# Optimization experiments

Hardware: AMD Instinct MI355X
Metric: run time of the kernel (lower is better)

## Reference

```python
import jax, jax.numpy as jnp
import numpy as np

N_NODES = 50000
N_EDGES = 800000
HEADS = 5
NFEAT = 5
C1 = 32  # hidden_layers


def setup_inputs() -> dict:
    key = jax.random.key(0)
    ks = jax.random.split(key, 20)
    s = 0.3  # glorot-ish scale
    d = {
        "x": jax.random.normal(ks[0], (N_NODES, NFEAT), jnp.float32),
        "edge_attr": jax.random.uniform(ks[1], (N_EDGES, 1), jnp.float32),
        "src": jax.random.randint(ks[2], (N_EDGES,), 0, N_NODES, jnp.int32),
        "dst": jax.random.randint(ks[3], (N_EDGES,), 0, N_NODES, jnp.int32),
        # conv1: in=5 -> heads=5, out=32, concat
        "W1": jax.random.normal(ks[4], (NFEAT, HEADS * C1), jnp.float32) * s,
        "a_src1": jax.random.normal(ks[5], (HEADS, C1), jnp.float32) * s,
        "a_dst1": jax.random.normal(ks[6], (HEADS, C1), jnp.float32) * s,
        "We1": jax.random.normal(ks[7], (1, HEADS * C1), jnp.float32) * s,
        "ae1": jax.random.normal(ks[8], (HEADS, C1), jnp.float32) * s,
        "b1": jnp.zeros((HEADS * C1,), jnp.float32),
        # conv2: in=160 -> heads=5, out=1, mean over heads
        "W2": jax.random.normal(ks[9], (HEADS * C1, HEADS * 1), jnp.float32) * 0.08,
        "a_src2": jax.random.normal(ks[10], (HEADS, 1), jnp.float32) * s,
        "a_dst2": jax.random.normal(ks[11], (HEADS, 1), jnp.float32) * s,
        "We2": jax.random.normal(ks[12], (1, HEADS * 1), jnp.float32) * s,
        "ae2": jax.random.normal(ks[13], (HEADS, 1), jnp.float32) * s,
        "b2": jnp.zeros((1,), jnp.float32),
        "Wlin": jax.random.normal(ks[14], (1, 1), jnp.float32),
    }
    return d


def gat_layer(x, src, dst, eattr, W, a_src, a_dst, We, a_e, bias, concat, n_nodes):
    """PyG GATConv with edge_dim, self-loops already added by caller."""
    H, C = a_src.shape
    h = (x @ W).reshape(-1, H, C)                      # [N,H,C]
    alpha_s = (h * a_src[None]).sum(-1)                # [N,H]
    alpha_d = (h * a_dst[None]).sum(-1)                # [N,H]
    ee = (eattr @ We).reshape(-1, H, C)                # [E,H,C]
    alpha_e = (ee * a_e[None]).sum(-1)                 # [E,H]
    logits = jax.nn.leaky_relu(alpha_s[src] + alpha_d[dst] + alpha_e, 0.2)
    # segment softmax over destination nodes
    m = jax.ops.segment_max(logits, dst, num_segments=n_nodes)
    m = jnp.where(jnp.isfinite(m), m, 0.0)
    ex = jnp.exp(logits - m[dst])
    denom = jax.ops.segment_sum(ex, dst, num_segments=n_nodes)
    alpha = ex / (denom[dst] + 1e-16)                  # [E,H]
    msg = (alpha[:, :, None] * h[src]).reshape(-1, H * C)
    agg = jax.ops.segment_sum(msg, dst, num_segments=n_nodes).reshape(n_nodes, H, C)
    if concat:
        return agg.reshape(n_nodes, H * C) + bias
    return agg.mean(axis=1) + bias


def reference(x, edge_attr, src, dst, W1, a_src1, a_dst1, We1, ae1, b1,
              W2, a_src2, a_dst2, We2, ae2, b2, Wlin):
    n = x.shape[0]
    loop = jnp.arange(n, dtype=src.dtype)
    s = jnp.concatenate([src, loop])
    t = jnp.concatenate([dst, loop])
    # self-loop edge_attr = mean of edge_attr (PyG fill_value='mean')
    ea_loop = jnp.broadcast_to(edge_attr.mean(axis=0, keepdims=True), (n, edge_attr.shape[1]))
    ea = jnp.concatenate([edge_attr, ea_loop], axis=0)

    x1 = gat_layer(x, s, t, ea, W1, a_src1, a_dst1, We1, ae1, b1, True, n)
    x2 = jax.nn.relu(x1)
    # dropout p=0.2 is identity in eval mode
    x4 = gat_layer(x2, s, t, ea, W2, a_src2, a_dst2, We2, ae2, b2, False, n)
    x5 = x4 @ Wlin                                     # Linear(1,1,bias=False)
    return jax.nn.sigmoid(x5)                          # [N,1]
```

## Files before the change

kernel.cpp:

```cpp
#include <hip/hip_runtime.h>
#include <hip/hip_fp16.h>
#include <math.h>

#define N_NODES 50000
#define N_EDGES 800000
#define E2 (N_EDGES + N_NODES)
#define HEADS 5
#define C1 32
#define F1 160

#define BSZ 64
#define NBK 782
#define NBL 128
#define CH  6641
#define MTOT (NBK*NBL)
#define MC  391
#define GRID_H1 (N_NODES/4)
#define CAP 1408

static constexpr size_t alignup(size_t x){ return (x + 255) & ~size_t(255); }
static constexpr size_t OFF_SCAL  = 0;
static constexpr size_t OFF_H     = alignup(OFF_SCAL + 64*4);
static constexpr size_t OFF_EAS   = alignup(OFF_H    + (size_t)MTOT*4);
static constexpr size_t OFF_PART  = alignup(OFF_EAS  + (size_t)NBL*4);
static constexpr size_t OFF_PPREF = alignup(OFF_PART + (size_t)MC*4);
static constexpr size_t OFF_BST   = alignup(OFF_PPREF+ (size_t)MC*4);
static constexpr size_t OFF_OFFS  = alignup(OFF_BST  + (size_t)(NBK+1)*4);
static constexpr size_t OFF_BPACK = alignup(OFF_OFFS + (size_t)(N_NODES+1)*4);
static constexpr size_t OFF_EDG   = alignup(OFF_BPACK+ (size_t)E2*8);
static constexpr size_t OFF_AS1P  = alignup(OFF_EDG  + (size_t)E2*4);
static constexpr size_t OFF_AD1P  = alignup(OFF_AS1P + (size_t)N_NODES*8*4);
static constexpr size_t OFF_G16   = alignup(OFF_AD1P + (size_t)N_NODES*8*4);
static constexpr size_t OFF_AD2P  = alignup(OFF_G16  + (size_t)N_NODES*16*2);
static constexpr size_t OFF_H1Q   = alignup(OFF_AD2P + (size_t)N_NODES*8*4);
static constexpr size_t OFF_X2H   = alignup(OFF_H1Q  + (size_t)N_NODES*F1);

typedef float vf2 __attribute__((ext_vector_type(2)));
__device__ __forceinline__ float4 fp8x4_to_f32(unsigned int r){
  vf2 lo = __builtin_amdgcn_cvt_pk_f32_fp8((int)r, false);
  vf2 hi = __builtin_amdgcn_cvt_pk_f32_fp8((int)r, true);
  return make_float4(lo.x, lo.y, hi.x, hi.y);
}

__global__ __launch_bounds__(320) void k_init(const float* __restrict__ x, const float* __restrict__ W1,
                       const float* __restrict__ as1w, const float* __restrict__ ad1w,
                       unsigned short* __restrict__ h1q, float* __restrict__ as1p, float* __restrict__ ad1p,
                       const int* __restrict__ dst, const float* __restrict__ ea,
                       int* __restrict__ H, float* __restrict__ easum){
  __shared__ float sW[5*F1];
  int t = threadIdx.x;
  if (blockIdx.x < GRID_H1){
    for (int k = t; k < 5*F1; k += 320) sW[k] = W1[k];
    __syncthreads();
    int nl = t / 80;
    int c  = t - nl*80;
    int n  = blockIdx.x*4 + nl;
    int c0 = 2*c;
    float hv0 = 0.f, hv1 = 0.f;
    #pragma unroll
    for (int f = 0; f < 5; f++){
      float xv = x[n*5 + f];
      hv0 += xv * sW[f*F1 + c0];
      hv1 += xv * sW[f*F1 + c0 + 1];
    }
    int pk = __builtin_amdgcn_cvt_pk_fp8_f32(hv0, hv1, 0, false);
    h1q[n*80 + c] = (unsigned short)(pk & 0xFFFF);
    float vs = hv0*as1w[c0] + hv1*as1w[c0+1];
    float vd = hv0*ad1w[c0] + hv1*ad1w[c0+1];
    #pragma unroll
    for (int m = 8; m >= 1; m >>= 1){
      vs += __shfl_xor(vs, m, 64);
      vd += __shfl_xor(vd, m, 64);
    }
    if ((c & 15) == 0){
      int h = c >> 4;
      as1p[n*8 + h] = vs;
      ad1p[n*8 + h] = vd;
    }
  } else {
    int* hist = (int*)sW;
    float* wsum = (float*)&hist[NBK + 1];
    for (int k = t; k < NBK; k += 320) hist[k] = 0;
    __syncthreads();
    int b = blockIdx.x - GRID_H1;
    int e0 = b*CH, e1 = min(e0 + CH, E2);
    float s = 0.f;
    for (int e = e0 + t; e < e1; e += 320){
      int d;
      if (e < N_EDGES){ d = dst[e]; s += ea[e]; }
      else d = e - N_EDGES;
      atomicAdd(&hist[d >> 6], 1);
    }
    #pragma unroll
    for (int m = 1; m < 64; m <<= 1) s += __shfl_xor(s, m, 64);
    if ((t & 63) == 0) wsum[t >> 6] = s;
    __syncthreads();
    for (int k = t; k < NBK; k += 320) H[(size_t)k*NBL + b] = hist[k];
    if (t == 0) easum[b] = wsum[0] + wsum[1] + wsum[2] + wsum[3] + wsum[4];
  }
}

__global__ void k_s1(const int* __restrict__ H, int* __restrict__ partial){
  int i = blockIdx.x*256 + threadIdx.x;
  int v = (i < MTOT) ? H[i] : 0;
  #pragma unroll
  for (int m = 1; m < 64; m <<= 1) v += __shfl_xor(v, m, 64);
  __shared__ int sh[4];
  if ((threadIdx.x & 63) == 0) sh[threadIdx.x >> 6] = v;
  __syncthreads();
  if (threadIdx.x == 0) partial[blockIdx.x] = sh[0] + sh[1] + sh[2] + sh[3];
}

__global__ __launch_bounds__(512) void k_s2p(const int* __restrict__ partial, int* __restrict__ ppref,
                      int* __restrict__ offs, int* __restrict__ bstart,
                      const float* __restrict__ easum,
                      const float* __restrict__ We1, const float* __restrict__ ae1,
                      const float* __restrict__ We2, const float* __restrict__ ae2,
                      float* __restrict__ scal){
  __shared__ int sp[512];
  __shared__ float sh_ea[NBL];
  int t = threadIdx.x;
  if (t < NBL) sh_ea[t] = easum[t];
  if (t >= 448 && t < 448 + HEADS){
    int h = t - 448;
    float s = 0.f;
    for (int c = 0; c < C1; c++) s += We1[h*C1 + c] * ae1[h*C1 + c];
    scal[2 + h] = s;
    scal[7 + h] = We2[h] * ae2[h];
  }
  int v = (t < MC) ? partial[t] : 0;
  sp[t] = v;
  __syncthreads();
  if (t == 511){
    float es = 0.f;
    for (int i = 0; i < NBL; i++) es += sh_ea[i];
    scal[1] = es / (float)N_EDGES;
  }
  for (int off = 1; off < 512; off <<= 1){
    int u = (t >= off) ? sp[t - off] : 0;
    __syncthreads();
    sp[t] += u;
    __syncthreads();
  }
  if (t < MC) ppref[t] = sp[t] - v;
  if (t == 0){ offs[N_NODES] = E2; bstart[NBK] = E2; }
}

__global__ void k_s3(int* __restrict__ H, const int* __restrict__ ppref, int* __restrict__ bstart){
  __shared__ int sp[256];
  int b = blockIdx.x, t = threadIdx.x;
  int i = b*256 + t;
  int v = (i < MTOT) ? H[i] : 0;
  sp[t] = v;
  __syncthreads();
  for (int off = 1; off < 256; off <<= 1){
    int u = (t >= off) ? sp[t - off] : 0;
    __syncthreads();
    sp[t] += u;
    __syncthreads();
  }
  int P = ppref[b] + sp[t] - v;
  if (i < MTOT){
    H[i] = P;
    if (i % NBL == 0) bstart[i / NBL] = P;
  }
}

__global__ __launch_bounds__(256) void k_scat(const int* __restrict__ src, const int* __restrict__ dst,
                       const float* __restrict__ ea, const float* __restrict__ scal,
                       const int* __restrict__ H, int2* __restrict__ bpack){
  __shared__ int lofs[NBK];
  int b = blockIdx.x;
  for (int k = threadIdx.x; k < NBK; k += 256) lofs[k] = H[(size_t)k*NBL + b];
  __syncthreads();
  float mean = scal[1];
  int e0 = b*CH, e1 = min(e0 + CH, E2);
  for (int e = e0 + threadIdx.x; e < e1; e += 256){
    int d, s; float a;
    if (e < N_EDGES){ d = dst[e]; s = src[e]; a = ea[e]; }
    else { d = s = e - N_EDGES; a = mean; }
    int pos = atomicAdd(&lofs[d >> 6], 1);
    bpack[pos] = make_int2(s | ((d & 63) << 16), __float_as_int(a));
  }
}

__global__ __launch_bounds__(256) void k_final2(const int* __restrict__ bstart,
                        const int2* __restrict__ bpack,
                        int* __restrict__ offs, unsigned int* __restrict__ edge2){
  __shared__ int cnt[BSZ], cur[BSZ];
  __shared__ unsigned int s_edge[CAP];
  int k = blockIdx.x, t = threadIdx.x;
  int base = k*BSZ;
  if (t < BSZ) cnt[t] = 0;
  __syncthreads();
  int r0 = bstart[k], r1 = bstart[k + 1];
  int sz = r1 - r0;
  for (int j = r0 + t; j < r1; j += 256) atomicAdd(&cnt[(bpack[j].x >> 16) & 63], 1);
  __syncthreads();
  if (t == 0){
    int run = 0;
    for (int i = 0; i < BSZ; i++){ int c = cnt[i]; cnt[i] = run; cur[i] = run; run += c; }
  }
  __syncthreads();
  if (t < BSZ){
    int n = base + t;
    if (n < N_NODES) offs[n] = r0 + cnt[t];
  }
  if (sz <= CAP){
    for (int j = r0 + t; j < r1; j += 256){
      int2 v = bpack[j];
      int lp = atomicAdd(&cur[(v.x >> 16) & 63], 1);
      s_edge[lp] = (unsigned int)(v.x & 0xFFFF) |
                   ((unsigned int)__half_as_ushort(__float2half(__int_as_float(v.y))) << 16);
    }
    __syncthreads();
    for (int i = t; i < sz; i += 256) edge2[r0 + i] = s_edge[i];
  } else {
    for (int j = r0 + t; j < r1; j += 256){
      int2 v = bpack[j];
      int pos = r0 + atomicAdd(&cur[(v.x >> 16) & 63], 1);
      edge2[pos] = (unsigned int)(v.x & 0xFFFF) |
                   ((unsigned int)__half_as_ushort(__float2half(__int_as_float(v.y))) << 16);
    }
  }
}

__global__ __launch_bounds__(320) void k_agg1(const int* __restrict__ offs,
                      const unsigned int* __restrict__ edge2,
                      const float* __restrict__ as1p, const float* __restrict__ ad1p,
                      const float* __restrict__ scal,
                      const unsigned short* __restrict__ h1q,
                      const float* __restrict__ b1, __half* __restrict__ x2h){
  int nl = threadIdx.x / 40;
  int c4 = threadIdx.x - nl*40;
  int n  = blockIdx.x*8 + nl;
  int h  = c4 >> 3;
  float wd  = scal[2 + h];
  float adn = ad1p[n*8 + h];
  const unsigned int* h1row = (const unsigned int*)h1q;
  int j0 = offs[n], j1 = offs[n + 1];
  float a0 = 0.f, a1 = 0.f, a2 = 0.f, a3 = 0.f, den = 0.f;
  int j = j0;
  for (; j + 7 < j1; j += 8){
    uint4 sa = *(const uint4*)(edge2 + j);
    uint4 sb = *(const uint4*)(edge2 + j + 4);
    unsigned int e0 = sa.x, e1 = sa.y, e2v = sa.z, e3 = sa.w;
    unsigned int e4 = sb.x, e5 = sb.y, e6 = sb.z, e7 = sb.w;
    int s0 = e0 & 0xFFFF, s1 = e1 & 0xFFFF, s2 = e2v & 0xFFFF, s3 = e3 & 0xFFFF;
    int s4 = e4 & 0xFFFF, s5 = e5 & 0xFFFF, s6 = e6 & 0xFFFF, s7 = e7 & 0xFFFF;
    unsigned int r0 = h1row[(size_t)s0*40 + c4];
    unsigned int r1 = h1row[(size_t)s1*40 + c4];
    unsigned int r2 = h1row[(size_t)s2*40 + c4];
    unsigned int r3 = h1row[(size_t)s3*40 + c4];
    unsigned int r4 = h1row[(size_t)s4*40 + c4];
    unsigned int r5 = h1row[(size_t)s5*40 + c4];
    unsigned int r6 = h1row[(size_t)s6*40 + c4];
    unsigned int r7 = h1row[(size_t)s7*40 + c4];
    float g0 = as1p[s0*8 + h], g1 = as1p[s1*8 + h];
    float g2 = as1p[s2*8 + h], g3 = as1p[s3*8 + h];
    float g4 = as1p[s4*8 + h], g5 = as1p[s5*8 + h];
    float g6 = as1p[s6*8 + h], g7 = as1p[s7*8 + h];
    float c0 = __half2float(__ushort_as_half((unsigned short)(e0 >> 16)));
    float c1 = __half2float(__ushort_as_half((unsigned short)(e1 >> 16)));
    float c2 = __half2float(__ushort_as_half((unsigned short)(e2v >> 16)));
    float c3 = __half2float(__ushort_as_half((unsigned short)(e3 >> 16)));
    float c4v = __half2float(__ushort_as_half((unsigned short)(e4 >> 16)));
    float c5v = __half2float(__ushort_as_half((unsigned short)(e5 >> 16)));
    float c6 = __half2float(__ushort_as_half((unsigned short)(e6 >> 16)));
    float c7 = __half2float(__ushort_as_half((unsigned short)(e7 >> 16)));
    float l0 = g0 + adn + c0*wd;  l0 = fminf(fmaxf(l0, 0.2f*l0), 10.f);
    float l1 = g1 + adn + c1*wd;  l1 = fminf(fmaxf(l1, 0.2f*l1), 10.f);
    float l2 = g2 + adn + c2*wd;  l2 = fminf(fmaxf(l2, 0.2f*l2), 10.f);
    float l3 = g3 + adn + c3*wd;  l3 = fminf(fmaxf(l3, 0.2f*l3), 10.f);
    float l4 = g4 + adn + c4v*wd; l4 = fminf(fmaxf(l4, 0.2f*l4), 10.f);
    float l5 = g5 + adn + c5v*wd; l5 = fminf(fmaxf(l5, 0.2f*l5), 10.f);
    float l6 = g6 + adn + c6*wd;  l6 = fminf(fmaxf(l6, 0.2f*l6), 10.f);
    float l7 = g7 + adn + c7*wd;  l7 = fminf(fmaxf(l7, 0.2f*l7), 10.f);
    float p0 = __expf(l0), p1 = __expf(l1), p2 = __expf(l2), p3 = __expf(l3);
    float p4 = __expf(l4), p5 = __expf(l5), p6 = __expf(l6), p7 = __expf(l7);
    den += p0 + p1 + p2 + p3 + p4 + p5 + p6 + p7;
    float4 f0 = fp8x4_to_f32(r0), f1 = fp8x4_to_f32(r1);
    float4 f2 = fp8x4_to_f32(r2), f3 = fp8x4_to_f32(r3);
    float4 f4 = fp8x4_to_f32(r4), f5 = fp8x4_to_f32(r5);
    float4 f6 = fp8x4_to_f32(r6), f7 = fp8x4_to_f32(r7);
    a0 += p0*f0.x; a1 += p0*f0.y; a2 += p0*f0.z; a3 += p0*f0.w;
    a0 += p1*f1.x; a1 += p1*f1.y; a2 += p1*f1.z; a3 += p1*f1.w;
    a0 += p2*f2.x; a1 += p2*f2.y; a2 += p2*f2.z; a3 += p2*f2.w;
    a0 += p3*f3.x; a1 += p3*f3.y; a2 += p3*f3.z; a3 += p3*f3.w;
    a0 += p4*f4.x; a1 += p4*f4.y; a2 += p4*f4.z; a3 += p4*f4.w;
    a0 += p5*f5.x; a1 += p5*f5.y; a2 += p5*f5.z; a3 += p5*f5.w;
    a0 += p6*f6.x; a1 += p6*f6.y; a2 += p6*f6.z; a3 += p6*f6.w;
    a0 += p7*f7.x; a1 += p7*f7.y; a2 += p7*f7.z; a3 += p7*f7.w;
  }
  for (; j < j1; ++j){
    unsigned int e = edge2[j];
    int s = e & 0xFFFF;
    float c = __half2float(__ushort_as_half((unsigned short)(e >> 16)));
    float g = as1p[s*8 + h];
    float lg = g + adn + c*wd;
    lg = fminf(fmaxf(lg, 0.2f*lg), 10.f);
    float p = __expf(lg);
    den += p;
    float4 f = fp8x4_to_f32(h1row[(size_t)s*40 + c4]);
    a0 += p*f.x; a1 += p*f.y; a2 += p*f.z; a3 += p*f.w;
  }
  float inv = 1.f / (den + 1e-16f);
  float4 bb = *(const float4*)(b1 + 4*c4);
  float v0 = fmaxf(a0*inv + bb.x, 0.f);
  float v1 = fmaxf(a1*inv + bb.y, 0.f);
  float v2 = fmaxf(a2*inv + bb.z, 0.f);
  float v3 = fmaxf(a3*inv + bb.w, 0.f);
  __half2 o0 = __floats2half2_rn(v0, v1);
  __half2 o1 = __floats2half2_rn(v2, v3);
  *(uint2*)(x2h + (size_t)n*F1 + 4*c4) =
      make_uint2(*(unsigned int*)&o0, *(unsigned int*)&o1);
}

__global__ __launch_bounds__(256) void k_h2(const __half* __restrict__ x2h, const float* __restrict__ W2,
                    const float* __restrict__ asw2, const float* __restrict__ adw2,
                    __half* __restrict__ G16, float* __restrict__ ad2p){
  __shared__ float sW[F1*HEADS];
  for (int k = threadIdx.x; k < F1*HEADS; k += 256) sW[k] = W2[k];
  __syncthreads();
  int w = threadIdx.x >> 6, l = threadIdx.x & 63;
  int n = blockIdx.x*4 + w;
  const __half2* x22 = (const __half2*)x2h;
  float acc[HEADS] = {0.f, 0.f, 0.f, 0.f, 0.f};
  for (int k2 = l; k2 < 80; k2 += 64){
    float2 f = __half22float2(x22[(size_t)n*80 + k2]);
    #pragma unroll
    for (int h = 0; h < HEADS; h++)
      acc[h] += f.x * sW[(2*k2)*HEADS + h] + f.y * sW[(2*k2+1)*HEADS + h];
  }
  #pragma unroll
  for (int m = 1; m < 64; m <<= 1){
    #pragma unroll
    for (int h = 0; h < HEADS; h++) acc[h] += __shfl_xor(acc[h], m, 64);
  }
  if (l == 0){
    #pragma unroll
    for (int h = 0; h < HEADS; h++){
      G16[(size_t)n*16 + h]     = __float2half(acc[h]);
      G16[(size_t)n*16 + 5 + h] = __float2half(acc[h] * asw2[h]);
      ad2p[n*8 + h]             = acc[h] * adw2[h];
    }
    #pragma unroll
    for (int z = 10; z < 16; z++) G16[(size_t)n*16 + z] = __float2half(0.f);
  }
}

__global__ __launch_bounds__(256) void k_agg2(const int* __restrict__ offs,
                      const unsigned int* __restrict__ edge2,
                      const __half* __restrict__ G16, const float* __restrict__ ad2p,
                      const float* __restrict__ scal,
                      const float* __restrict__ b2, const float* __restrict__ Wlin,
                      float* __restrict__ out){
  int grp = threadIdx.x >> 4;
  int l16 = threadIdx.x & 15;
  int n = blockIdx.x*16 + grp;
  float adn[HEADS], wd[HEADS];
  #pragma unroll
  for (int h = 0; h < HEADS; h++){ adn[h] = ad2p[n*8 + h]; wd[h] = scal[7 + h]; }
  int j0 = offs[n], j1 = offs[n + 1];

  float den[HEADS] = {0,0,0,0,0};
  float ac[HEADS]  = {0,0,0,0,0};
  for (int j = j0 + l16; j < j1; j += 16){
    unsigned int e = edge2[j];
    int s = e & 0xFFFF;
    float c = __half2float(__ushort_as_half((unsigned short)(e >> 16)));
    const __half* gs = G16 + (size_t)s*16;
    union { uint4 u; __half2 h[4]; } U; U.u = *(const uint4*)gs;
    union { uint2 u; __half2 h[2]; } V; V.u = *(const uint2*)(gs + 8);
    float2 p01 = __half22float2(U.h[0]);
    float2 p23 = __half22float2(U.h[1]);
    float2 p45 = __half22float2(U.h[2]);
    float2 p67 = __half22float2(U.h[3]);
    float2 p89 = __half22float2(V.h[0]);
    float hv[HEADS] = {p01.x, p01.y, p23.x, p23.y, p45.x};
    float av[HEADS] = {p45.y, p67.x, p67.y, p89.x, p89.y};
    #pragma unroll
    for (int h = 0; h < HEADS; h++){
      float lg = av[h] + adn[h] + c*wd[h];
      lg = fmaxf(lg, 0.2f*lg);
      lg = fminf(lg, 50.f);
      float p = __expf(lg);
      den[h] += p;
      ac[h]  += p * hv[h];
    }
  }
  #pragma unroll
  for (int m = 1; m < 16; m <<= 1){
    #pragma unroll
    for (int h = 0; h < HEADS; h++){
      den[h] += __shfl_xor(den[h], m, 16);
      ac[h]  += __shfl_xor(ac[h], m, 16);
    }
  }
  if (l16 == 0){
    float v = 0.f;
    #pragma unroll
    for (int h = 0; h < HEADS; h++) v += ac[h] / (den[h] + 1e-16f);
    v = v * (1.f/HEADS) + b2[0];
    v *= Wlin[0];
    out[n] = 1.f / (1.f + __expf(-v));
  }
}

extern "C" void kernel_launch(void* const* d_in, const int* in_sizes, int n_in,
                              void* d_out, int out_size, void* d_ws, size_t ws_size,
                              hipStream_t stream) {
  const float* x    = (const float*)d_in[0];
  const float* ea   = (const float*)d_in[1];
  const int*   src  = (const int*)d_in[2];
  const int*   dst  = (const int*)d_in[3];
  const float* W1   = (const float*)d_in[4];
  const float* as1w = (const float*)d_in[5];
  const float* ad1w = (const float*)d_in[6];
  const float* We1  = (const float*)d_in[7];
  const float* ae1  = (const float*)d_in[8];
  const float* b1   = (const float*)d_in[9];
  const float* W2   = (const float*)d_in[10];
  const float* as2w = (const float*)d_in[11];
  const float* ad2w = (const float*)d_in[12];
  const float* We2  = (const float*)d_in[13];
  const float* ae2  = (const float*)d_in[14];
  const float* b2   = (const float*)d_in[15];
  const float* Wlin = (const float*)d_in[16];

  char* ws = (char*)d_ws;
  float* scal   = (float*)(ws + OFF_SCAL);
  int*   H      = (int*)  (ws + OFF_H);
  float* easum  = (float*)(ws + OFF_EAS);
  int*   part   = (int*)  (ws + OFF_PART);
  int*   ppref  = (int*)  (ws + OFF_PPREF);
  int*   bstart = (int*)  (ws + OFF_BST);
  int*   offs   = (int*)  (ws + OFF_OFFS);
  int2*  bpack  = (int2*) (ws + OFF_BPACK);
  unsigned int* edge2 = (unsigned int*)(ws + OFF_EDG);
  float* as1p   = (float*)(ws + OFF_AS1P);
  float* ad1p   = (float*)(ws + OFF_AD1P);
  __half* G16   = (__half*)(ws + OFF_G16);
  float* ad2p   = (float*)(ws + OFF_AD2P);
  unsigned short* h1q = (unsigned short*)(ws + OFF_H1Q);
  __half* x2h   = (__half*)(ws + OFF_X2H);
  float* outp   = (float*)d_out;

  k_init   <<<GRID_H1 + NBL, 320, 0, stream>>>(x, W1, as1w, ad1w, h1q, as1p, ad1p,
                                               dst, ea, H, easum);
  k_s1     <<<MC, 256, 0, stream>>>(H, part);
  k_s2p    <<<1, 512, 0, stream>>>(part, ppref, offs, bstart, easum, We1, ae1, We2, ae2, scal);
  k_s3     <<<MC, 256, 0, stream>>>(H, ppref, bstart);
  k_scat   <<<NBL, 256, 0, stream>>>(src, dst, ea, scal, H, bpack);
  k_final2 <<<NBK, 256, 0, stream>>>(bstart, bpack, offs, edge2);

  k_agg1   <<<N_NODES/8, 320, 0, stream>>>(offs, edge2, as1p, ad1p, scal, h1q, b1, x2h);
  k_h2     <<<N_NODES/4, 256, 0, stream>>>(x2h, W2, as2w, ad2w, G16, ad2p);
  k_agg2   <<<N_NODES/16, 256, 0, stream>>>(offs, edge2, G16, ad2p, scal, b2, Wlin, outp);
}
```

Measured before the change: 225.8 us.

## Split layer-1 aggregation per head with head-major feature layout

Stores the fp8 layer-1 features and the per-node source/destination attention scores in head-major layout, and launches the first aggregation kernel as a separate grid slice per head. Each group of 8 threads handles one node for one head. The goal is a smaller gathered working set per slice (32 bytes per source row plus a dense score array) for better cache locality on random source gathers. In exchange, each node's edge list and edge attributes are read five times, once per head.

```diff
diff --git a/kernel.cpp b/kernel.cpp
--- a/kernel.cpp
+++ b/kernel.cpp
@@ -17,6 +17,9 @@
 #define MC  391
 #define GRID_H1 (N_NODES/4)
 #define CAP 1408
+
+#define AGG1_NPB 32
+#define AGG1_NB  1563
 
 static constexpr size_t alignup(size_t x){ return (x + 255) & ~size_t(255); }
 static constexpr size_t OFF_SCAL  = 0;
@@ -44,7 +47,7 @@
 
 __global__ __launch_bounds__(320) void k_init(const float* __restrict__ x, const float* __restrict__ W1,
                        const float* __restrict__ as1w, const float* __restrict__ ad1w,
-                       unsigned short* __restrict__ h1q, float* __restrict__ as1p, float* __restrict__ ad1p,
+                       unsigned short* __restrict__ h1qh, float* __restrict__ as1ph, float* __restrict__ ad1ph,
                        const int* __restrict__ dst, const float* __restrict__ ea,
                        int* __restrict__ H, float* __restrict__ easum){
   __shared__ float sW[5*F1];
@@ -64,7 +67,8 @@
       hv1 += xv * sW[f*F1 + c0 + 1];
     }
     int pk = __builtin_amdgcn_cvt_pk_fp8_f32(hv0, hv1, 0, false);
-    h1q[n*80 + c] = (unsigned short)(pk & 0xFFFF);
+    int hh = c >> 4, pp = c & 15;
+    h1qh[(size_t)hh*(N_NODES*16) + n*16 + pp] = (unsigned short)(pk & 0xFFFF);
     float vs = hv0*as1w[c0] + hv1*as1w[c0+1];
     float vd = hv0*ad1w[c0] + hv1*ad1w[c0+1];
     #pragma unroll
@@ -74,8 +78,8 @@
     }
     if ((c & 15) == 0){
       int h = c >> 4;
-      as1p[n*8 + h] = vs;
-      ad1p[n*8 + h] = vd;
+      as1ph[h*N_NODES + n] = vs;
+      ad1ph[h*N_NODES + n] = vd;
     }
   } else {
     int* hist = (int*)sW;
@@ -225,19 +229,22 @@
   }
 }
 
-__global__ __launch_bounds__(320) void k_agg1(const int* __restrict__ offs,
+__global__ __launch_bounds__(256) void k_agg1(const int* __restrict__ offs,
                       const unsigned int* __restrict__ edge2,
-                      const float* __restrict__ as1p, const float* __restrict__ ad1p,
+                      const float* __restrict__ as1ph, const float* __restrict__ ad1ph,
                       const float* __restrict__ scal,
-                      const unsigned short* __restrict__ h1q,
+                      const unsigned short* __restrict__ h1qh,
                       const float* __restrict__ b1, __half* __restrict__ x2h){
-  int nl = threadIdx.x / 40;
-  int c4 = threadIdx.x - nl*40;
-  int n  = blockIdx.x*8 + nl;
-  int h  = c4 >> 3;
-  float wd  = scal[2 + h];
-  float adn = ad1p[n*8 + h];
-  const unsigned int* h1row = (const unsigned int*)h1q;
+  int head = blockIdx.x / AGG1_NB;
+  int nb   = blockIdx.x - head*AGG1_NB;
+  int gl   = threadIdx.x >> 3;
+  int q    = threadIdx.x & 7;
+  int n    = nb*AGG1_NPB + gl;
+  if (n >= N_NODES) return;
+  float wd  = scal[2 + head];
+  float adn = ad1ph[head*N_NODES + n];
+  const float* asn = as1ph + head*N_NODES;
+  const unsigned int* h1row = (const unsigned int*)h1qh + (size_t)head*(N_NODES*8) + q;
   int j0 = offs[n], j1 = offs[n + 1];
   float a0 = 0.f, a1 = 0.f, a2 = 0.f, a3 = 0.f, den = 0.f;
   int j = j0;
@@ -248,18 +255,18 @@
     unsigned int e4 = sb.x, e5 = sb.y, e6 = sb.z, e7 = sb.w;
     int s0 = e0 & 0xFFFF, s1 = e1 & 0xFFFF, s2 = e2v & 0xFFFF, s3 = e3 & 0xFFFF;
     int s4 = e4 & 0xFFFF, s5 = e5 & 0xFFFF, s6 = e6 & 0xFFFF, s7 = e7 & 0xFFFF;
-    unsigned int r0 = h1row[(size_t)s0*40 + c4];
-    unsigned int r1 = h1row[(size_t)s1*40 + c4];
-    unsigned int r2 = h1row[(size_t)s2*40 + c4];
-    unsigned int r3 = h1row[(size_t)s3*40 + c4];
-    unsigned int r4 = h1row[(size_t)s4*40 + c4];
-    unsigned int r5 = h1row[(size_t)s5*40 + c4];
-    unsigned int r6 = h1row[(size_t)s6*40 + c4];
-    unsigned int r7 = h1row[(size_t)s7*40 + c4];
-    float g0 = as1p[s0*8 + h], g1 = as1p[s1*8 + h];
-    float g2 = as1p[s2*8 + h], g3 = as1p[s3*8 + h];
-    float g4 = as1p[s4*8 + h], g5 = as1p[s5*8 + h];
-    float g6 = as1p[s6*8 + h], g7 = as1p[s7*8 + h];
+    unsigned int r0 = h1row[s0*8];
+    unsigned int r1 = h1row[s1*8];
+    unsigned int r2 = h1row[s2*8];
+    unsigned int r3 = h1row[s3*8];
+    unsigned int r4 = h1row[s4*8];
+    unsigned int r5 = h1row[s5*8];
+    unsigned int r6 = h1row[s6*8];
+    unsigned int r7 = h1row[s7*8];
+    float g0 = asn[s0], g1 = asn[s1];
+    float g2 = asn[s2], g3 = asn[s3];
+    float g4 = asn[s4], g5 = asn[s5];
+    float g6 = asn[s6], g7 = asn[s7];
     float c0 = __half2float(__ushort_as_half((unsigned short)(e0 >> 16)));
     float c1 = __half2float(__ushort_as_half((unsigned short)(e1 >> 16)));
     float c2 = __half2float(__ushort_as_half((unsigned short)(e2v >> 16)));
@@ -296,23 +303,23 @@
     unsigned int e = edge2[j];
     int s = e & 0xFFFF;
     float c = __half2float(__ushort_as_half((unsigned short)(e >> 16)));
-    float g = as1p[s*8 + h];
+    float g = asn[s];
     float lg = g + adn + c*wd;
     lg = fminf(fmaxf(lg, 0.2f*lg), 10.f);
     float p = __expf(lg);
     den += p;
-    float4 f = fp8x4_to_f32(h1row[(size_t)s*40 + c4]);
+    float4 f = fp8x4_to_f32(h1row[s*8]);
     a0 += p*f.x; a1 += p*f.y; a2 += p*f.z; a3 += p*f.w;
   }
   float inv = 1.f / (den + 1e-16f);
-  float4 bb = *(const float4*)(b1 + 4*c4);
+  float4 bb = *(const float4*)(b1 + head*C1 + 4*q);
   float v0 = fmaxf(a0*inv + bb.x, 0.f);
   float v1 = fmaxf(a1*inv + bb.y, 0.f);
   float v2 = fmaxf(a2*inv + bb.z, 0.f);
   float v3 = fmaxf(a3*inv + bb.w, 0.f);
   __half2 o0 = __floats2half2_rn(v0, v1);
   __half2 o1 = __floats2half2_rn(v2, v3);
-  *(uint2*)(x2h + (size_t)n*F1 + 4*c4) =
+  *(uint2*)(x2h + (size_t)n*F1 + head*C1 + 4*q) =
       make_uint2(*(unsigned int*)&o0, *(unsigned int*)&o1);
 }
 
@@ -438,15 +445,15 @@
   int*   offs   = (int*)  (ws + OFF_OFFS);
   int2*  bpack  = (int2*) (ws + OFF_BPACK);
   unsigned int* edge2 = (unsigned int*)(ws + OFF_EDG);
-  float* as1p   = (float*)(ws + OFF_AS1P);
-  float* ad1p   = (float*)(ws + OFF_AD1P);
+  float* as1ph  = (float*)(ws + OFF_AS1P);
+  float* ad1ph  = (float*)(ws + OFF_AD1P);
   __half* G16   = (__half*)(ws + OFF_G16);
   float* ad2p   = (float*)(ws + OFF_AD2P);
-  unsigned short* h1q = (unsigned short*)(ws + OFF_H1Q);
+  unsigned short* h1qh = (unsigned short*)(ws + OFF_H1Q);
   __half* x2h   = (__half*)(ws + OFF_X2H);
   float* outp   = (float*)d_out;
 
-  k_init   <<<GRID_H1 + NBL, 320, 0, stream>>>(x, W1, as1w, ad1w, h1q, as1p, ad1p,
+  k_init   <<<GRID_H1 + NBL, 320, 0, stream>>>(x, W1, as1w, ad1w, h1qh, as1ph, ad1ph,
                                                dst, ea, H, easum);
   k_s1     <<<MC, 256, 0, stream>>>(H, part);
   k_s2p    <<<1, 512, 0, stream>>>(part, ppref, offs, bstart, easum, We1, ae1, We2, ae2, scal);
@@ -454,7 +461,7 @@
   k_scat   <<<NBL, 256, 0, stream>>>(src, dst, ea, scal, H, bpack);
   k_final2 <<<NBK, 256, 0, stream>>>(bstart, bpack, offs, edge2);
 
-  k_agg1   <<<N_NODES/8, 320, 0, stream>>>(offs, edge2, as1p, ad1p, scal, h1q, b1, x2h);
+  k_agg1   <<<HEADS*AGG1_NB, 256, 0, stream>>>(offs, edge2, as1ph, ad1ph, scal, h1qh, b1, x2h);
   k_h2     <<<N_NODES/4, 256, 0, stream>>>(x2h, W2, as2w, ad2w, G16, ad2p);
   k_agg2   <<<N_NODES/16, 256, 0, stream>>>(offs, edge2, G16, ad2p, scal, b2, Wlin, outp);
 }
```

New measurement: 225.9 us. No clear change (+0.0%).
